# Kernel optimization log

Hardware: AMD Instinct MI355X
Metric: run time of the kernel (lower is better)

The kernel has to match this reference:

```python
import jax, jax.numpy as jnp
import numpy as np

# Dims. NOTE: TransmorpherLayer2d passes (dim_head, num_heads) positionally into an
# attention class whose signature is (num_heads, dim_head) -> attention runs with
# H = dim_head = 64 heads of size Dh = num_heads = 12. embed_dim D = 768 either way.
B, S, L = 1, 64, 512
H, Dh = 64, 12
D = H * Dh          # 768
DFF = 3072
EPS = 1e-5


def _ln(x, g, b):
    m = x.mean(-1, keepdims=True)
    v = ((x - m) ** 2).mean(-1, keepdims=True)
    return (x - m) / jnp.sqrt(v + EPS) * g + b


def setup_inputs() -> dict:
    key = jax.random.key(0)
    ks = jax.random.split(key, 6)
    sd = 0.02
    p = {
        'x': jax.random.normal(ks[0], (B, S, L, D), jnp.float32),
        'w_row': jax.random.normal(ks[1], (D, 3 * D), jnp.float32) * sd,
        'b_row': jnp.zeros((3 * D,), jnp.float32),
        'w_col': jax.random.normal(ks[2], (D, 3 * D), jnp.float32) * sd,
        'b_col': jnp.zeros((3 * D,), jnp.float32),
        'g_a1': jnp.ones((D,), jnp.float32), 'be_a1': jnp.zeros((D,), jnp.float32),
        'g_a2': jnp.ones((D,), jnp.float32), 'be_a2': jnp.zeros((D,), jnp.float32),
        'w1': jax.random.normal(ks[3], (D, DFF), jnp.float32) * sd,
        'b1f': jnp.zeros((DFF,), jnp.float32),
        'w2': jax.random.normal(ks[4], (DFF, D), jnp.float32) * sd,
        'b2f': jnp.zeros((D,), jnp.float32),
        'g_n1': jnp.ones((D,), jnp.float32), 'be_n1': jnp.zeros((D,), jnp.float32),
        'g_n2': jnp.ones((D,), jnp.float32), 'be_n2': jnp.zeros((D,), jnp.float32),
    }
    return p


def reference(x, w_row, b_row, w_col, b_col, g_a1, be_a1, g_a2, be_a2,
              w1, b1f, w2, b2f, g_n1, be_n1, g_n2, be_n2):
    def qkv(t, w, b):
        q, k, v = jnp.split(t @ w + b, 3, axis=-1)
        rs = lambda a: a.reshape(B, S, L, H, Dh)
        return rs(q), rs(k), rs(v)

    # ---- TiedAxialSelfAttention2d (no 1/sqrt(d) scaling, tied over S) ----
    q, k, v = qkv(x, w_row, b_row)
    row_attn = jax.nn.softmax(jnp.einsum('bsihc,bsjhc->bhij', q, k), axis=-1)  # [B,H,L,L]
    row_out = jnp.einsum('bhij,bsjhd->bsihd', row_attn, v).reshape(B, S, L, D)
    out = _ln(x + row_out, g_a1, be_a1)

    q, k, v = qkv(out, w_col, b_col)
    col_attn = jax.nn.softmax(jnp.einsum('bilhc,bjlhc->bhijl', q, k), axis=-2)  # [B,H,S,S,L]
    col_out = jnp.einsum('bhijl,bjlhd->bilhd', col_attn, v).reshape(B, S, L, D)
    out = _ln(out + col_out, g_a2, be_a2)

    # ---- TransmorpherLayer2d residual + FFN (post-LN) ----
    y = _ln(x + out, g_n1, be_n1)
    ff = jax.nn.relu(y @ w1 + b1f) @ w2 + b2f
    return _ln(y + ff, g_n2, be_n2)
```

## Files before the change

### kernel.cpp

```cpp
#include <hip/hip_runtime.h>

typedef unsigned short u16;
typedef unsigned int u32;
typedef __attribute__((ext_vector_type(8))) short short8;
typedef __attribute__((ext_vector_type(4))) float floatx4;

#define LN_EPS 1e-5f
#define REG 6291456L

__device__ __forceinline__ float b2f(u16 u) {
    return __builtin_bit_cast(float, (u32)u << 16);
}
__device__ __forceinline__ u16 f2b(float f) {
    u32 x = __builtin_bit_cast(u32, f);
    return (u16)((x + 0x7fffu + ((x >> 16) & 1u)) >> 16);
}

__device__ __forceinline__ void gload16(const u16* g, u16* l) {
    __builtin_amdgcn_global_load_lds(
        (const __attribute__((address_space(1))) void*)g,
        (__attribute__((address_space(3))) void*)l, 16, 0, 0);
}

template<int BN_, int EPI, int RELU, int HASBIAS, int SMAJ>
__global__ __launch_bounds__(256, 2) void gemm_dma(
    const u16* __restrict__ A, const u16* __restrict__ BT,
    const float* __restrict__ bias, void* __restrict__ C,
    int Nb, int K, long sA, long sB, long sC, int colbase)
{
    constexpr int NCH = (128 + BN_) / 64;
    constexpr int JF  = BN_ / 32;
    __shared__ u16 lds[(128 + BN_) * 32];

    const u16* Az = A + (long)blockIdx.z * sA;
    const u16* Bz = BT + (long)blockIdx.z * sB;
    const int n0 = blockIdx.x * BN_;
    const int tid = threadIdx.x;
    const int lane = tid & 63;
    const int wm = ((tid >> 6) >> 1) * 64;
    const int wn = ((tid >> 6) & 1) * (BN_ / 2);
    const int lrow = lane & 15;
    const int quad = lane >> 4;

    floatx4 acc[4][JF];
#pragma unroll
    for (int i = 0; i < 4; i++)
#pragma unroll
        for (int j = 0; j < JF; j++)
            acc[i][j] = (floatx4){0.f, 0.f, 0.f, 0.f};

    for (int kt = 0; kt < K; kt += 32) {
#pragma unroll
        for (int it = 0; it < NCH; it++) {
            const int idx = tid + it * 256;
            const u16* src;
            if (idx < 512) {
                const int row = idx >> 2;
                const int ch  = (idx & 3) * 8;
                const long grow = SMAJ
                    ? ((long)(row >> 1) * 512 + (blockIdx.y << 1) + (row & 1))
                    : ((long)blockIdx.y * 128 + row);
                src = Az + grow * K + kt + ch;
            } else {
                const int bidx = idx - 512;
                const int row = bidx >> 2;
                const int ch  = (bidx & 3) * 8;
                src = Bz + (long)(n0 + row) * K + kt + ch;
            }
            gload16(src, &lds[idx * 8]);
        }
        __syncthreads();

        short8 af[4], bfr[JF];
#pragma unroll
        for (int i = 0; i < 4; i++)
            af[i] = *(const short8*)&lds[(wm + i * 16 + lrow) * 32 + quad * 8];
#pragma unroll
        for (int j = 0; j < JF; j++)
            bfr[j] = *(const short8*)&lds[4096 + (wn + j * 16 + lrow) * 32 + quad * 8];
#pragma unroll
        for (int i = 0; i < 4; i++)
#pragma unroll
            for (int j = 0; j < JF; j++)
                acc[i][j] = __builtin_amdgcn_mfma_f32_16x16x32_bf16(
                    af[i], bfr[j], acc[i][j], 0, 0, 0);
        __syncthreads();
    }

    const int z = blockIdx.z;
#pragma unroll
    for (int j = 0; j < JF; j++) {
        const int n = n0 + wn + j * 16 + lrow;
        int t = 0, jj = n;
        if (EPI == 8 || EPI == 9) { t = n / 192; jj = n - t * 192; }
        const int hl = jj / 12;
        const int cc = jj - hl * 12;
        float bv = 0.f;
        if (HASBIAS)
            bv = (EPI == 8 || EPI == 9) ? bias[t * 768 + colbase + jj]
                                        : bias[colbase + n];
#pragma unroll
        for (int i = 0; i < 4; i++) {
            const int mb = wm + i * 16 + quad * 4;
#pragma unroll
            for (int r = 0; r < 4; r++) {
                const int ml = mb + r;
                float v = acc[i][j][r] + bv;
                if (RELU) v = fmaxf(v, 0.f);
                if (EPI == 0) {
                    const long m = (long)blockIdx.y * 128 + ml;
                    ((u16*)C)[m * Nb + n] = f2b(v);
                } else if (EPI == 1) {
                    const long m = (long)blockIdx.y * 128 + ml;
                    ((float*)C)[(long)z * sC + m * Nb + n] = v;
                } else if (EPI == 3) {
                    const int gm = blockIdx.y * 128 + ml;
                    const int s = gm >> 9, iL = gm & 511;
                    ((u16*)C)[(long)hl * 393216 + (long)(s * 12 + cc) * 512 + iL] = f2b(v);
                } else if (EPI == 4) {
                    const int m = blockIdx.y * 128 + ml;
                    ((u16*)C)[((long)hl * 512 + m) * 768 + colbase + z * 12 + cc] = f2b(v);
                } else if (EPI == 8) {
                    const int s = ml >> 1, iL = (blockIdx.y << 1) + (ml & 1);
                    ((u16*)C)[(long)t * REG + ((long)hl * 512 + iL) * 768 + s * 12 + cc] = f2b(v);
                } else if (EPI == 9) {
                    const int s = ml >> 1, l = (blockIdx.y << 1) + (ml & 1);
                    ((u16*)C)[(long)t * REG + (long)hl * 393216 + (long)l * 768 + s * 12 + cc] = f2b(v);
                }
            }
        }
    }
}

__global__ __launch_bounds__(256) void cast_kernel(
    const float* __restrict__ X, u16* __restrict__ Xb)
{
    const long i = ((long)blockIdx.x * 256 + threadIdx.x) * 8;
    float4 a = *(const float4*)(X + i);
    float4 b = *(const float4*)(X + i + 4);
    u16 t8[8] = { f2b(a.x), f2b(a.y), f2b(a.z), f2b(a.w),
                  f2b(b.x), f2b(b.y), f2b(b.z), f2b(b.w) };
    *(uint4*)(Xb + i) = *(const uint4*)t8;
}

__global__ __launch_bounds__(256) void transpose_kernel(
    const float* __restrict__ In, u16* __restrict__ Out, int R, int Ccols)
{
    __shared__ u16 tile[32][33];
    int tx = threadIdx.x & 31;
    int ty = threadIdx.x >> 5;
    int c0 = blockIdx.x * 32;
    int r0 = blockIdx.y * 32;
#pragma unroll
    for (int rr = 0; rr < 32; rr += 8)
        tile[ty + rr][tx] = f2b(In[(long)(r0 + ty + rr) * Ccols + c0 + tx]);
    __syncthreads();
#pragma unroll
    for (int rr = 0; rr < 32; rr += 8)
        Out[(long)(c0 + ty + rr) * R + r0 + tx] = tile[tx][ty + rr];
}

__global__ __launch_bounds__(256) void pack_qk_kernel(
    const float* __restrict__ In, u16* __restrict__ Out)
{
    __shared__ u16 tile[32][33];
    int tx = threadIdx.x & 31;
    int ty = threadIdx.x >> 5;
    int p0 = blockIdx.x * 32;
    int k0 = blockIdx.y * 32;
    int hg = p0 / 384, rem = p0 % 384;
    int t = rem / 192, j0 = rem % 192;
    int c0 = t * 768 + hg * 192 + j0;
#pragma unroll
    for (int rr = 0; rr < 32; rr += 8)
        tile[ty + rr][tx] = f2b(In[(long)(k0 + ty + rr) * 2304 + c0 + tx]);
    __syncthreads();
#pragma unroll
    for (int rr = 0; rr < 32; rr += 8)
        Out[(long)(p0 + ty + rr) * 768 + k0 + tx] = tile[tx][ty + rr];
}

__global__ __launch_bounds__(256) void pack_v_kernel(
    const float* __restrict__ In, u16* __restrict__ Out)
{
    __shared__ u16 tile[32][33];
    int tx = threadIdx.x & 31;
    int ty = threadIdx.x >> 5;
    int p0 = blockIdx.x * 32;
    int k0 = blockIdx.y * 32;
    int hg = p0 / 192, j0 = p0 % 192;
    int c0 = 1536 + hg * 192 + j0;
#pragma unroll
    for (int rr = 0; rr < 32; rr += 8)
        tile[ty + rr][tx] = f2b(In[(long)(k0 + ty + rr) * 2304 + c0 + tx]);
    __syncthreads();
#pragma unroll
    for (int rr = 0; rr < 32; rr += 8)
        Out[(long)(p0 + ty + rr) * 768 + k0 + tx] = tile[tx][ty + rr];
}

__global__ __launch_bounds__(256) void qkv_pack_kernel(
    const float* __restrict__ In, u16* __restrict__ Out)
{
    __shared__ u16 tile[32][33];
    int tx = threadIdx.x & 31;
    int ty = threadIdx.x >> 5;
    int p0 = blockIdx.x * 32;
    int k0 = blockIdx.y * 32;
    int hg = p0 / 576, r0 = p0 % 576;
    int t = r0 / 192, j0 = r0 % 192;
    int c0 = t * 768 + hg * 192 + j0;
#pragma unroll
    for (int rr = 0; rr < 32; rr += 8)
        tile[ty + rr][tx] = f2b(In[(long)(k0 + ty + rr) * 2304 + c0 + tx]);
    __syncthreads();
#pragma unroll
    for (int rr = 0; rr < 32; rr += 8)
        Out[(long)(p0 + ty + rr) * 768 + k0 + tx] = tile[tx][ty + rr];
}

__global__ __launch_bounds__(256) void softmax_kernel(
    const float* __restrict__ S, u16* __restrict__ P)
{
    const long r = blockIdx.x;
    const float* sp = S + r * 512;
    int t = threadIdx.x;
    float a = sp[t], b = sp[t + 256];
    __shared__ float red[256];
    red[t] = fmaxf(a, b);
    __syncthreads();
    for (int o = 128; o > 0; o >>= 1) {
        if (t < o) red[t] = fmaxf(red[t], red[t + o]);
        __syncthreads();
    }
    float mx = red[0];
    __syncthreads();
    float ea = __expf(a - mx), eb = __expf(b - mx);
    red[t] = ea + eb;
    __syncthreads();
    for (int o = 128; o > 0; o >>= 1) {
        if (t < o) red[t] += red[t + o];
        __syncthreads();
    }
    float inv = 1.0f / red[0];
    P[r * 512 + t] = f2b(ea * inv);
    P[r * 512 + t + 256] = f2b(eb * inv);
}

template<int AF, int BF, int OF>
__global__ __launch_bounds__(256) void ln_add_kernel(
    const void* __restrict__ Xa, const void* __restrict__ Xb,
    const float* __restrict__ g, const float* __restrict__ be,
    void* __restrict__ Out)
{
    const long r = blockIdx.x;
    int t = threadIdx.x;
    float v[3]; float sm = 0.f, s2 = 0.f;
#pragma unroll
    for (int e = 0; e < 3; e++) {
        long c = r * 768 + t + e * 256;
        float xa = AF ? ((const float*)Xa)[c] : b2f(((const u16*)Xa)[c]);
        float xb = BF ? ((const float*)Xb)[c] : b2f(((const u16*)Xb)[c]);
        float x = xa + xb;
        v[e] = x; sm += x; s2 += x * x;
    }
    __shared__ float r1[256], r2[256];
    r1[t] = sm; r2[t] = s2;
    __syncthreads();
    for (int o = 128; o > 0; o >>= 1) {
        if (t < o) { r1[t] += r1[t + o]; r2[t] += r2[t + o]; }
        __syncthreads();
    }
    float mean = r1[0] * (1.0f / 768.0f);
    float var  = r2[0] * (1.0f / 768.0f) - mean * mean;
    float rstd = rsqrtf(var + LN_EPS);
#pragma unroll
    for (int e = 0; e < 3; e++) {
        int c = t + e * 256;
        float o = (v[e] - mean) * rstd * g[c] + be[c];
        if (OF) ((float*)Out)[r * 768 + c] = o;
        else    ((u16*)Out)[r * 768 + c] = f2b(o);
    }
}

__global__ __launch_bounds__(256) void ln_ln_kernel(
    const u16* __restrict__ A, const u16* __restrict__ B,
    const float* __restrict__ X,
    const float* __restrict__ g1, const float* __restrict__ be1,
    const float* __restrict__ g2, const float* __restrict__ be2,
    float* __restrict__ Out, u16* __restrict__ Outb)
{
    const long r = blockIdx.x;
    int t = threadIdx.x;
    __shared__ float r1[256], r2[256];

    float u[3]; float sm = 0.f, s2 = 0.f;
#pragma unroll
    for (int e = 0; e < 3; e++) {
        long c = r * 768 + t + e * 256;
        float x = b2f(A[c]) + b2f(B[c]);
        u[e] = x; sm += x; s2 += x * x;
    }
    r1[t] = sm; r2[t] = s2;
    __syncthreads();
    for (int o = 128; o > 0; o >>= 1) {
        if (t < o) { r1[t] += r1[t + o]; r2[t] += r2[t + o]; }
        __syncthreads();
    }
    float mean1 = r1[0] * (1.0f / 768.0f);
    float var1  = r2[0] * (1.0f / 768.0f) - mean1 * mean1;
    float rstd1 = rsqrtf(var1 + LN_EPS);
    __syncthreads();

    float w[3]; sm = 0.f; s2 = 0.f;
#pragma unroll
    for (int e = 0; e < 3; e++) {
        int c = t + e * 256;
        float tv = (u[e] - mean1) * rstd1 * g1[c] + be1[c];
        float wv = X[r * 768 + c] + tv;
        w[e] = wv; sm += wv; s2 += wv * wv;
    }
    r1[t] = sm; r2[t] = s2;
    __syncthreads();
    for (int o = 128; o > 0; o >>= 1) {
        if (t < o) { r1[t] += r1[t + o]; r2[t] += r2[t + o]; }
        __syncthreads();
    }
    float mean2 = r1[0] * (1.0f / 768.0f);
    float var2  = r2[0] * (1.0f / 768.0f) - mean2 * mean2;
    float rstd2 = rsqrtf(var2 + LN_EPS);
#pragma unroll
    for (int e = 0; e < 3; e++) {
        int c = t + e * 256;
        float o = (w[e] - mean2) * rstd2 * g2[c] + be2[c];
        Out[r * 768 + c] = o;
        Outb[r * 768 + c] = f2b(o);
    }
}

__global__ __launch_bounds__(64) void col_attn_kernel(
    const u16* __restrict__ qc, const u16* __restrict__ kc,
    const u16* __restrict__ vc, u16* __restrict__ Out, int hbase)
{
    const int hh = blockIdx.x >> 9;
    const int l  = blockIdx.x & 511;
    const int i  = threadIdx.x;
    const long base = ((long)hh * 512 + l) * 768;
    __shared__ float Ks[64][12];
    __shared__ float Vs[64][12];
    float q[12];
#pragma unroll
    for (int c = 0; c < 12; c++) {
        q[c] = b2f(qc[base + i * 12 + c]);
        Ks[i][c] = b2f(kc[base + i * 12 + c]);
        Vs[i][c] = b2f(vc[base + i * 12 + c]);
    }
    __syncthreads();
    float sc[64];
#pragma unroll
    for (int j = 0; j < 64; j++) {
        float a = 0.f;
#pragma unroll
        for (int c = 0; c < 12; c++) a += q[c] * Ks[j][c];
        sc[j] = a;
    }
    float m = sc[0];
#pragma unroll
    for (int j = 1; j < 64; j++) m = fmaxf(m, sc[j]);
    float sum = 0.f;
#pragma unroll
    for (int j = 0; j < 64; j++) { sc[j] = __expf(sc[j] - m); sum += sc[j]; }
    float inv = 1.0f / sum;
    float o[12];
#pragma unroll
    for (int c = 0; c < 12; c++) o[c] = 0.f;
#pragma unroll
    for (int j = 0; j < 64; j++) {
        float p = sc[j] * inv;
#pragma unroll
        for (int c = 0; c < 12; c++) o[c] += p * Vs[j][c];
    }
    u16* op = Out + ((long)i * 512 + l) * 768 + hbase + hh * 12;
#pragma unroll
    for (int c = 0; c < 12; c++) op[c] = f2b(o[c]);
}

extern "C" void kernel_launch(void* const* d_in, const int* in_sizes, int n_in,
                              void* d_out, int out_size, void* d_ws, size_t ws_size,
                              hipStream_t stream)
{
    (void)in_sizes; (void)n_in; (void)out_size; (void)ws_size;

    const float* x     = (const float*)d_in[0];
    const float* w_row = (const float*)d_in[1];
    const float* b_row = (const float*)d_in[2];
    const float* w_col = (const float*)d_in[3];
    const float* b_col = (const float*)d_in[4];
    const float* g_a1  = (const float*)d_in[5];
    const float* be_a1 = (const float*)d_in[6];
    const float* g_a2  = (const float*)d_in[7];
    const float* be_a2 = (const float*)d_in[8];
    const float* w1    = (const float*)d_in[9];
    const float* b1f   = (const float*)d_in[10];
    const float* w2    = (const float*)d_in[11];
    const float* b2f_  = (const float*)d_in[12];
    const float* g_n1  = (const float*)d_in[13];
    const float* be_n1 = (const float*)d_in[14];
    const float* g_n2  = (const float*)d_in[15];
    const float* be_n2 = (const float*)d_in[16];
    float* outp = (float*)d_out;

    char* wp = (char*)d_ws;
    auto alloc = [&](size_t bytes) -> void* {
        void* p = (void*)wp;
        wp += (bytes + 255) & ~(size_t)255;
        return p;
    };
    u16*   wPqk   = (u16*)alloc((size_t)1536 * 768 * 2);
    u16*   wPv    = (u16*)alloc((size_t)768 * 768 * 2);
    u16*   wPcol  = (u16*)alloc((size_t)2304 * 768 * 2);
    u16*   w1T    = (u16*)alloc((size_t)3072 * 768 * 2);
    u16*   w2T    = (u16*)alloc((size_t)768 * 3072 * 2);
    u16*   bufA   = (u16*)alloc((size_t)32768 * 768 * 2);
    u16*   bufB   = (u16*)alloc((size_t)32768 * 768 * 2);
    u16*   qkvg   = (u16*)alloc((size_t)3 * 16 * 512 * 768 * 2);
    float* scores = (float*)alloc((size_t)16 * 512 * 512 * 4);
    u16*   probs  = (u16*)alloc((size_t)16 * 512 * 512 * 2);
    u16*   hidden = qkvg;
    u16*   xb     = bufB;
    u16*   ybf    = bufB;
    float* y      = outp;

    pack_qk_kernel<<<dim3(48, 24), 256, 0, stream>>>(w_row, wPqk);
    pack_v_kernel<<<dim3(24, 24), 256, 0, stream>>>(w_row, wPv);
    qkv_pack_kernel<<<dim3(72, 24), 256, 0, stream>>>(w_col, wPcol);
    transpose_kernel<<<dim3(96, 24), 256, 0, stream>>>(w1, w1T, 768, 3072);
    transpose_kernel<<<dim3(24, 96), 256, 0, stream>>>(w2, w2T, 3072, 768);
    cast_kernel<<<12288, 256, 0, stream>>>(x, xb);

    for (int hg = 0; hg < 4; hg++) {
        gemm_dma<192, 8, 0, 1, 1><<<dim3(2, 256), 256, 0, stream>>>(
            xb, wPqk + (long)hg * 384 * 768, b_row, qkvg,
            384, 768, 0, 0, 0, hg * 192);
        gemm_dma<192, 3, 0, 1, 0><<<dim3(1, 256), 256, 0, stream>>>(
            xb, wPv + (long)hg * 192 * 768, b_row, qkvg + 2 * REG,
            192, 768, 0, 0, 0, 1536 + hg * 192);
        gemm_dma<128, 1, 0, 0, 0><<<dim3(4, 4, 16), 256, 0, stream>>>(
            qkvg, qkvg + REG, nullptr, scores,
            512, 768, (long)512 * 768, (long)512 * 768, (long)512 * 512, 0);
        softmax_kernel<<<8192, 256, 0, stream>>>(scores, probs);
        gemm_dma<128, 4, 0, 0, 0><<<dim3(6, 4, 16), 256, 0, stream>>>(
            probs, qkvg + 2 * REG, nullptr, bufA,
            768, 512, (long)512 * 512, (long)768 * 512, 0, hg * 192);
    }
    ln_add_kernel<1, 0, 0><<<32768, 256, 0, stream>>>(x, bufA, g_a1, be_a1, bufB);

    for (int hg = 0; hg < 4; hg++) {
        gemm_dma<192, 9, 0, 1, 1><<<dim3(3, 256), 256, 0, stream>>>(
            bufB, wPcol + (long)hg * 576 * 768, b_col, qkvg,
            576, 768, 0, 0, 0, hg * 192);
        col_attn_kernel<<<8192, 64, 0, stream>>>(
            qkvg, qkvg + REG, qkvg + 2 * REG, bufA, hg * 192);
    }
    ln_ln_kernel<<<32768, 256, 0, stream>>>(
        bufB, bufA, x, g_a2, be_a2, g_n1, be_n1, y, ybf);

    for (int mc = 0; mc < 4; mc++) {
        const long off = (long)mc * 8192 * 768;
        gemm_dma<192, 0, 1, 1, 0><<<dim3(16, 64), 256, 0, stream>>>(
            ybf + off, w1T, b1f, hidden, 3072, 768, 0, 0, 0, 0);
        gemm_dma<192, 0, 0, 1, 0><<<dim3(4, 64), 256, 0, stream>>>(
            hidden, w2T, b2f_, bufA + off, 768, 3072, 0, 0, 0, 0);
    }
    ln_add_kernel<1, 0, 1><<<32768, 256, 0, stream>>>(y, bufA, g_n2, be_n2, outp);
}
```

Before: 1.784 ms.

## Fuse row-attention scores, softmax and PV into a single flash-style kernel

Replaces the per-head-group sequence of a scores GEMM, a separate softmax kernel and a PV GEMM with one kernel. Each block computes a 32x512 score tile in registers, does the softmax with cross-wave reductions through shared memory, writes bf16 probabilities to LDS, and multiplies them by V read directly from global memory. This drops the fp32 score and bf16 probability round-trips through global memory and two kernel launches per head group. In exchange the grid shrinks to 256 blocks, and the K tile is reloaded for every 32-row query block, which may limit occupancy and reuse.

```diff
diff --git a/kernel.cpp b/kernel.cpp
--- a/kernel.cpp
+++ b/kernel.cpp
@@ -87,7 +87,6 @@
         __syncthreads();
     }
 
-    const int z = blockIdx.z;
 #pragma unroll
     for (int j = 0; j < JF; j++) {
         const int n = n0 + wn + j * 16 + lrow;
@@ -110,16 +109,10 @@
                 if (EPI == 0) {
                     const long m = (long)blockIdx.y * 128 + ml;
                     ((u16*)C)[m * Nb + n] = f2b(v);
-                } else if (EPI == 1) {
-                    const long m = (long)blockIdx.y * 128 + ml;
-                    ((float*)C)[(long)z * sC + m * Nb + n] = v;
                 } else if (EPI == 3) {
                     const int gm = blockIdx.y * 128 + ml;
                     const int s = gm >> 9, iL = gm & 511;
                     ((u16*)C)[(long)hl * 393216 + (long)(s * 12 + cc) * 512 + iL] = f2b(v);
-                } else if (EPI == 4) {
-                    const int m = blockIdx.y * 128 + ml;
-                    ((u16*)C)[((long)hl * 512 + m) * 768 + colbase + z * 12 + cc] = f2b(v);
                 } else if (EPI == 8) {
                     const int s = ml >> 1, iL = (blockIdx.y << 1) + (ml & 1);
                     ((u16*)C)[(long)t * REG + ((long)hl * 512 + iL) * 768 + s * 12 + cc] = f2b(v);
@@ -132,6 +125,140 @@
     }
 }
 
+__global__ __launch_bounds__(256, 2) void flash_row_kernel(
+    const u16* __restrict__ Qg, const u16* __restrict__ Kg,
+    const u16* __restrict__ Vt, u16* __restrict__ Out, int hbase)
+{
+    __shared__ __align__(16) u16 lds[17408];
+    __shared__ float pmx[2][32];
+    __shared__ float psm[2][32];
+
+    const int h  = blockIdx.y;
+    const int i0 = blockIdx.x * 32;
+    const u16* Qh = Qg + (long)h * 393216;
+    const u16* Kh = Kg + (long)h * 393216;
+    const u16* Vh = Vt + (long)h * 393216;
+    const int tid  = threadIdx.x;
+    const int w    = tid >> 6;
+    const int wr   = w >> 1;
+    const int wc   = w & 1;
+    const int lane = tid & 63;
+    const int lrow = lane & 15;
+    const int quad = lane >> 4;
+
+    floatx4 acc[16];
+#pragma unroll
+    for (int j = 0; j < 16; j++) acc[j] = (floatx4){0.f, 0.f, 0.f, 0.f};
+
+    for (int kt = 0; kt < 768; kt += 32) {
+        if (tid < 128) {
+            const int row = tid >> 2, ch = (tid & 3) * 8;
+            gload16(Qh + (long)(i0 + row) * 768 + kt + ch, &lds[tid * 8]);
+        } else {
+            const int b = tid - 128;
+            const int row = b >> 2, ch = (b & 3) * 8;
+            gload16(Kh + (long)row * 768 + kt + ch, &lds[tid * 8]);
+        }
+#pragma unroll
+        for (int it = 1; it < 8; it++) {
+            const int idx = tid + it * 256;
+            const int b = idx - 128;
+            const int row = b >> 2, ch = (b & 3) * 8;
+            gload16(Kh + (long)row * 768 + kt + ch, &lds[idx * 8]);
+        }
+        if (tid < 128) {
+            const int idx = tid + 2048;
+            const int b = idx - 128;
+            const int row = b >> 2, ch = (b & 3) * 8;
+            gload16(Kh + (long)row * 768 + kt + ch, &lds[idx * 8]);
+        }
+        __syncthreads();
+        const short8 af = *(const short8*)&lds[(wr * 16 + lrow) * 32 + quad * 8];
+#pragma unroll
+        for (int j = 0; j < 16; j++) {
+            const short8 bf = *(const short8*)
+                &lds[1024 + (wc * 256 + j * 16 + lrow) * 32 + quad * 8];
+            acc[j] = __builtin_amdgcn_mfma_f32_16x16x32_bf16(af, bf, acc[j], 0, 0, 0);
+        }
+        __syncthreads();
+    }
+
+    const int row32 = wr * 16 + quad * 4;
+    float pm[4], inv[4];
+#pragma unroll
+    for (int r = 0; r < 4; r++) {
+        float m = -3.0e38f;
+#pragma unroll
+        for (int j = 0; j < 16; j++) m = fmaxf(m, acc[j][r]);
+#pragma unroll
+        for (int d = 1; d < 16; d <<= 1) m = fmaxf(m, __shfl_xor(m, d));
+        pm[r] = m;
+        if (lrow == 0) pmx[wc][row32 + r] = m;
+    }
+    __syncthreads();
+#pragma unroll
+    for (int r = 0; r < 4; r++) {
+        const float m = fmaxf(pm[r], pmx[1 ^ wc][row32 + r]);
+        float s = 0.f;
+#pragma unroll
+        for (int j = 0; j < 16; j++) {
+            const float e = __expf(acc[j][r] - m);
+            acc[j][r] = e; s += e;
+        }
+#pragma unroll
+        for (int d = 1; d < 16; d <<= 1) s += __shfl_xor(s, d);
+        if (lrow == 0) psm[wc][row32 + r] = s;
+    }
+    __syncthreads();
+#pragma unroll
+    for (int r = 0; r < 4; r++)
+        inv[r] = 1.0f / (psm[0][row32 + r] + psm[1][row32 + r]);
+
+#pragma unroll
+    for (int j = 0; j < 16; j++)
+#pragma unroll
+        for (int r = 0; r < 4; r++)
+            lds[(row32 + r) * 520 + wc * 256 + j * 16 + lrow] =
+                f2b(acc[j][r] * inv[r]);
+    __syncthreads();
+
+    floatx4 acc2[2][12];
+#pragma unroll
+    for (int i = 0; i < 2; i++)
+#pragma unroll
+        for (int j = 0; j < 12; j++) acc2[i][j] = (floatx4){0.f, 0.f, 0.f, 0.f};
+
+    for (int kt2 = 0; kt2 < 512; kt2 += 32) {
+        short8 af2[2];
+#pragma unroll
+        for (int i = 0; i < 2; i++)
+            af2[i] = *(const short8*)&lds[(i * 16 + lrow) * 520 + kt2 + quad * 8];
+#pragma unroll
+        for (int j = 0; j < 12; j++) {
+            const int n = w * 192 + j * 16 + lrow;
+            const short8 bf = *(const short8*)(Vh + (long)n * 512 + kt2 + quad * 8);
+#pragma unroll
+            for (int i = 0; i < 2; i++)
+                acc2[i][j] = __builtin_amdgcn_mfma_f32_16x16x32_bf16(
+                    af2[i], bf, acc2[i][j], 0, 0, 0);
+        }
+    }
+
+#pragma unroll
+    for (int j = 0; j < 12; j++) {
+        const int n = w * 192 + j * 16 + lrow;
+        const int s = n / 12, d = n - (n / 12) * 12;
+#pragma unroll
+        for (int i = 0; i < 2; i++)
+#pragma unroll
+            for (int r = 0; r < 4; r++) {
+                const int m = i * 16 + quad * 4 + r;
+                Out[((long)s * 512 + i0 + m) * 768 + hbase + h * 12 + d] =
+                    f2b(acc2[i][j][r]);
+            }
+    }
+}
+
 __global__ __launch_bounds__(256) void cast_kernel(
     const float* __restrict__ X, u16* __restrict__ Xb)
 {
@@ -217,34 +344,6 @@
 #pragma unroll
     for (int rr = 0; rr < 32; rr += 8)
         Out[(long)(p0 + ty + rr) * 768 + k0 + tx] = tile[tx][ty + rr];
-}
-
-__global__ __launch_bounds__(256) void softmax_kernel(
-    const float* __restrict__ S, u16* __restrict__ P)
-{
-    const long r = blockIdx.x;
-    const float* sp = S + r * 512;
-    int t = threadIdx.x;
-    float a = sp[t], b = sp[t + 256];
-    __shared__ float red[256];
-    red[t] = fmaxf(a, b);
-    __syncthreads();
-    for (int o = 128; o > 0; o >>= 1) {
-        if (t < o) red[t] = fmaxf(red[t], red[t + o]);
-        __syncthreads();
-    }
-    float mx = red[0];
-    __syncthreads();
-    float ea = __expf(a - mx), eb = __expf(b - mx);
-    red[t] = ea + eb;
-    __syncthreads();
-    for (int o = 128; o > 0; o >>= 1) {
-        if (t < o) red[t] += red[t + o];
-        __syncthreads();
-    }
-    float inv = 1.0f / red[0];
-    P[r * 512 + t] = f2b(ea * inv);
-    P[r * 512 + t + 256] = f2b(eb * inv);
 }
 
 template<int AF, int BF, int OF>
@@ -423,9 +522,7 @@
     u16*   w2T    = (u16*)alloc((size_t)768 * 3072 * 2);
     u16*   bufA   = (u16*)alloc((size_t)32768 * 768 * 2);
     u16*   bufB   = (u16*)alloc((size_t)32768 * 768 * 2);
-    u16*   qkvg   = (u16*)alloc((size_t)3 * 16 * 512 * 768 * 2);
-    float* scores = (float*)alloc((size_t)16 * 512 * 512 * 4);
-    u16*   probs  = (u16*)alloc((size_t)16 * 512 * 512 * 2);
+    u16*   qkvg   = (u16*)alloc((size_t)8192 * 3072 * 2);
     u16*   hidden = qkvg;
     u16*   xb     = bufB;
     u16*   ybf    = bufB;
@@ -445,13 +542,8 @@
         gemm_dma<192, 3, 0, 1, 0><<<dim3(1, 256), 256, 0, stream>>>(
             xb, wPv + (long)hg * 192 * 768, b_row, qkvg + 2 * REG,
             192, 768, 0, 0, 0, 1536 + hg * 192);
-        gemm_dma<128, 1, 0, 0, 0><<<dim3(4, 4, 16), 256, 0, stream>>>(
-            qkvg, qkvg + REG, nullptr, scores,
-            512, 768, (long)512 * 768, (long)512 * 768, (long)512 * 512, 0);
-        softmax_kernel<<<8192, 256, 0, stream>>>(scores, probs);
-        gemm_dma<128, 4, 0, 0, 0><<<dim3(6, 4, 16), 256, 0, stream>>>(
-            probs, qkvg + 2 * REG, nullptr, bufA,
-            768, 512, (long)512 * 512, (long)768 * 512, 0, hg * 192);
+        flash_row_kernel<<<dim3(16, 16), 256, 0, stream>>>(
+            qkvg, qkvg + REG, qkvg + 2 * REG, bufA, hg * 192);
     }
     ln_add_kernel<1, 0, 0><<<32768, 256, 0, stream>>>(x, bufA, g_a1, be_a1, bufB);
 
```

After: 1.855 ms. 4.0% more time.
